# Kernel optimization log

Measured on AMD Instinct MI355X. Metric: run time of the kernel, lower is better.

Reference implementation:

```python
import jax, jax.numpy as jnp
import numpy as np

B, N, D = 2, 1024, 512
H, HD = 8, 64
RPE_IN, RPE_HID = 4, 64
FFN = 2048
EPS = 1e-5


def _layernorm(x, g, b):
    mu = jnp.mean(x, axis=-1, keepdims=True)
    var = jnp.var(x, axis=-1, keepdims=True)
    return (x - mu) * jax.lax.rsqrt(var + EPS) * g + b


def setup_inputs() -> dict:
    key = jax.random.key(0)
    ks = jax.random.split(key, 24)
    s = lambda fan_in: 1.0 / np.sqrt(fan_in)
    # weights stored [in, out] (torch Linear transposed)
    return {
        "x": jax.random.normal(ks[0], (B, N, D), jnp.float32),
        "rel_pos": jax.random.normal(ks[1], (B, N, N, RPE_IN), jnp.float32),
        "Wq": jax.random.uniform(ks[2], (D, D), jnp.float32, -s(D), s(D)),
        "bq": jnp.zeros((D,), jnp.float32),
        "Wk": jax.random.uniform(ks[3], (D, D), jnp.float32, -s(D), s(D)),
        "bk": jnp.zeros((D,), jnp.float32),
        "Wv": jax.random.uniform(ks[4], (D, D), jnp.float32, -s(D), s(D)),
        "bv": jnp.zeros((D,), jnp.float32),
        "Wo": jax.random.uniform(ks[5], (D, D), jnp.float32, -s(D), s(D)),
        "bo": jnp.zeros((D,), jnp.float32),
        "R1": jax.random.uniform(ks[6], (RPE_IN, RPE_HID), jnp.float32, -s(RPE_IN), s(RPE_IN)),
        "rb1": jnp.zeros((RPE_HID,), jnp.float32),
        "R2": jax.random.uniform(ks[7], (RPE_HID, H), jnp.float32, -s(RPE_HID), s(RPE_HID)),
        "rb2": jnp.zeros((H,), jnp.float32),
        "g1": jnp.ones((D,), jnp.float32),
        "b1": jnp.zeros((D,), jnp.float32),
        "g2": jnp.ones((D,), jnp.float32),
        "b2": jnp.zeros((D,), jnp.float32),
        "F1": jax.random.uniform(ks[8], (D, FFN), jnp.float32, -s(D), s(D)),
        "fb1": jnp.zeros((FFN,), jnp.float32),
        "F2": jax.random.uniform(ks[9], (FFN, D), jnp.float32, -s(FFN), s(FFN)),
        "fb2": jnp.zeros((D,), jnp.float32),
    }


def reference(x, rel_pos, Wq, bq, Wk, bk, Wv, bv, Wo, bo,
              R1, rb1, R2, rb2, g1, b1, g2, b2, F1, fb1, F2, fb2):
    scale = 1.0 / np.sqrt(HD)
    q = (x @ Wq + bq).reshape(B, N, H, HD).transpose(0, 2, 1, 3)  # [B,H,N,hd]
    k = (x @ Wk + bk).reshape(B, N, H, HD).transpose(0, 2, 1, 3)
    v = (x @ Wv + bv).reshape(B, N, H, HD).transpose(0, 2, 1, 3)
    attn = jnp.einsum('bhid,bhjd->bhij', q, k) * scale
    rpe = (jax.nn.relu(rel_pos @ R1 + rb1) @ R2 + rb2)  # [B,N,N,H]
    attn = attn + rpe.transpose(0, 3, 1, 2)
    attn = jax.nn.softmax(attn, axis=-1)
    out = jnp.einsum('bhij,bhjd->bhid', attn, v).transpose(0, 2, 1, 3).reshape(B, N, D)
    out = out @ Wo + bo
    x = _layernorm(x + out, g1, b1)
    ffn = jax.nn.gelu(x @ F1 + fb1, approximate=False) @ F2 + fb2
    return _layernorm(x + ffn, g2, b2)
```

## Files before the change

kernel.cpp:

```cpp
#include <hip/hip_runtime.h>
#include <math.h>

#define BATCH 2
#define SEQ   1024
#define DMODEL 512
#define NHEAD 8
#define HDIM  64
#define FFND  2048
#define BH    (BATCH*NHEAD)

typedef float  f32x4  __attribute__((ext_vector_type(4)));
typedef __bf16 bf16x8 __attribute__((ext_vector_type(8)));

#define WAITVM(n) asm volatile("s_waitcnt vmcnt(" #n ")" ::: "memory")

__device__ __forceinline__ unsigned short f2bf(float f) {
  union { __bf16 h; unsigned short u; } z; z.h = (__bf16)f; return z.u;
}
__device__ __forceinline__ float bf2f(unsigned short h) {
  union { unsigned u; float f; } x; x.u = ((unsigned)h) << 16;
  return x.f;
}
__device__ __forceinline__ unsigned pk2(float a, float b) {
  union { __bf16 h[2]; unsigned u; } z;
  z.h[0] = (__bf16)a; z.h[1] = (__bf16)b; return z.u;
}
__device__ __forceinline__ float gelu_f(float v) {
  float u = 0.7978845608f * (v + 0.044715f * v * v * v);
  float a = fabsf(u);
  float e = __expf(-2.f * a);
  float t = (1.f - e) / (1.f + e);
  t = copysignf(t, u);
  return 0.5f * v * (1.f + t);
}

__device__ __forceinline__ void load_lds16(const void* g, void* l) {
  __builtin_amdgcn_global_load_lds((const __attribute__((address_space(1))) void*)g,
                                   (__attribute__((address_space(3))) void*)l, 16, 0, 0);
}

__global__ __launch_bounds__(256) void prep_misc(
    const float* __restrict__ x, const float* __restrict__ bq,
    const float* __restrict__ bk, const float* __restrict__ bv,
    unsigned short* __restrict__ xb, float* __restrict__ bqkv) {
  int gid = blockIdx.x * 256 + threadIdx.x;
  float4 v = ((const float4*)x)[gid];
  ushort4 s;
  s.x = f2bf(v.x); s.y = f2bf(v.y); s.z = f2bf(v.z); s.w = f2bf(v.w);
  ((ushort4*)xb)[gid] = s;
  if (gid < 1536)
    bqkv[gid] = gid < 512 ? bq[gid] : (gid < 1024 ? bk[gid - 512] : bv[gid - 1024]);
}

__global__ __launch_bounds__(256) void prep_weights(
    const float* __restrict__ Wq, const float* __restrict__ Wk,
    const float* __restrict__ Wv, const float* __restrict__ Wo,
    const float* __restrict__ F1, const float* __restrict__ F2,
    unsigned short* __restrict__ qkvT, unsigned short* __restrict__ WoT,
    unsigned short* __restrict__ F1T, unsigned short* __restrict__ F2T) {
  __shared__ float t[32][33];
  int bid = blockIdx.x;
  const float* src; unsigned short* dst; int R, C, tx, ty;
  if (bid < 1024) {
    int m = bid >> 8;
    src = m == 0 ? Wq : m == 1 ? Wk : m == 2 ? Wv : Wo;
    dst = m < 3 ? qkvT + m * 512 * 512 : WoT;
    R = 512; C = 512; int u = bid & 255; tx = u & 15; ty = u >> 4;
  } else if (bid < 2048) {
    src = F1; dst = F1T; R = 512; C = 2048;
    int u = bid - 1024; tx = u & 63; ty = u >> 6;
  } else {
    src = F2; dst = F2T; R = 2048; C = 512;
    int u = bid - 2048; tx = u & 15; ty = u >> 4;
  }
  int c0 = tx * 32, r0 = ty * 32;
  int x_ = threadIdx.x, y_ = threadIdx.y;
#pragma unroll
  for (int i = 0; i < 4; i++)
    t[y_ + i * 8][x_] = src[(size_t)(r0 + y_ + i * 8) * C + c0 + x_];
  __syncthreads();
#pragma unroll
  for (int i = 0; i < 4; i++)
    dst[(size_t)(c0 + y_ + i * 8) * R + r0 + x_] = f2bf(t[x_][y_ + i * 8]);
}

__global__ __launch_bounds__(256) void rpe_mfma(
    const float* __restrict__ rel, const float* __restrict__ R1,
    const float* __restrict__ rb1, const float* __restrict__ R2,
    const float* __restrict__ rb2, unsigned short* __restrict__ rpe) {
  __shared__ unsigned short Hs[4][64 * 64];
  __shared__ unsigned short Os[4][8 * 64];
  const int tid = threadIdx.x, lane = tid & 63, w = tid >> 6;
  const int l15 = lane & 15, l4g = lane >> 4;
  char* Hw = (char*)&Hs[w][0];
  char* Ow = (char*)&Os[w][0];

  bf16x8 a1[4];
#pragma unroll
  for (int mt = 0; mt < 4; mt++) {
    bf16x8 z = {};
    if (l4g == 0) {
      int m = mt * 16 + l15;
      z[0] = (__bf16)R1[0 * 64 + m];
      z[1] = (__bf16)R1[1 * 64 + m];
      z[2] = (__bf16)R1[2 * 64 + m];
      z[3] = (__bf16)R1[3 * 64 + m];
      z[4] = (__bf16)rb1[m];
    }
    a1[mt] = z;
  }
  bf16x8 b2f[2];
#pragma unroll
  for (int ks = 0; ks < 2; ks++) {
    bf16x8 z = {};
    if (l15 < 8) {
#pragma unroll
      for (int j = 0; j < 8; j++)
        z[j] = (__bf16)R2[(ks * 32 + l4g * 8 + j) * 8 + l15];
    }
    b2f[ks] = z;
  }
  float rb2v = (l15 < 8) ? rb2[l15] : 0.f;

  const int nwaves = gridDim.x * 4;
  const int wgid = blockIdx.x * 4 + w;
  for (int itr = 0; itr < 8; itr++) {
    int p0 = (wgid + itr * nwaves) * 64;
    bf16x8 b1[4];
#pragma unroll
    for (int nt = 0; nt < 4; nt++) {
      bf16x8 z = {};
      if (l4g == 0) {
        float4 rv = *(const float4*)&rel[(size_t)(p0 + nt * 16 + l15) * 4];
        z[0] = (__bf16)rv.x; z[1] = (__bf16)rv.y;
        z[2] = (__bf16)rv.z; z[3] = (__bf16)rv.w;
        z[4] = (__bf16)1.0f;
      }
      b1[nt] = z;
    }
#pragma unroll
    for (int nt = 0; nt < 4; nt++) {
#pragma unroll
      for (int mt = 0; mt < 4; mt++) {
        f32x4 hacc = __builtin_amdgcn_mfma_f32_16x16x32_bf16(
            a1[mt], b1[nt], (f32x4){0.f, 0.f, 0.f, 0.f}, 0, 0, 0);
        int row = nt * 16 + l15;
        int dim0 = mt * 16 + l4g * 4;
        float v0 = fmaxf(hacc[0], 0.f);
        float v1 = fmaxf(hacc[1], 0.f);
        float v2 = fmaxf(hacc[2], 0.f);
        float v3 = fmaxf(hacc[3], 0.f);
        int byte = (row * 128 + dim0 * 2) ^ ((row & 7) << 4);
        uint2 pk; pk.x = pk2(v0, v1); pk.y = pk2(v2, v3);
        *(uint2*)(Hw + byte) = pk;
      }
    }
    f32x4 acc2[4];
#pragma unroll
    for (int mt = 0; mt < 4; mt++) acc2[mt] = (f32x4){0.f, 0.f, 0.f, 0.f};
#pragma unroll
    for (int ks = 0; ks < 2; ks++) {
#pragma unroll
      for (int mt = 0; mt < 4; mt++) {
        int row = mt * 16 + l15;
        int byte = (row * 128 + (ks * 32 + l4g * 8) * 2) ^ ((l15 & 7) << 4);
        bf16x8 af = *(const bf16x8*)(Hw + byte);
        acc2[mt] = __builtin_amdgcn_mfma_f32_16x16x32_bf16(af, b2f[ks], acc2[mt], 0, 0, 0);
      }
    }
#pragma unroll
    for (int mt = 0; mt < 4; mt++) {
      if (l15 < 8) {
        int byte = (l15 * 128 + (mt * 16 + l4g * 4) * 2) ^ ((l15 & 7) << 4);
        uint2 pk;
        pk.x = pk2(acc2[mt][0] + rb2v, acc2[mt][1] + rb2v);
        pk.y = pk2(acc2[mt][2] + rb2v, acc2[mt][3] + rb2v);
        *(uint2*)(Ow + byte) = pk;
      }
    }
    {
      int h = lane >> 3, rb = (lane & 7) * 8;
      int byte = (h * 128 + rb * 2) ^ ((h & 7) << 4);
      uint4 ov = *(const uint4*)(Ow + byte);
      int b = p0 >> 20, ij0 = (p0 & 1048575) + rb;
      *(uint4*)&rpe[((size_t)(b * 8 + h) << 20) + ij0] = ov;
    }
  }
}

enum { EPI_F32 = 0, EPI_GELU = 1, EPI_QKV = 2 };

template <int EPI, int BMt, int BNt, int WM, int WN>
__global__ __launch_bounds__(256) void gemm_bt(
    const unsigned short* __restrict__ A, const unsigned short* __restrict__ Bt,
    const float* __restrict__ bias, void* __restrict__ O0, void* __restrict__ O1,
    void* __restrict__ O2, int M, int N, int K) {
  __shared__ unsigned short As[2][BMt * 64];
  __shared__ unsigned short Bs[2][BNt * 64];
  const int tid = threadIdx.x, lane = tid & 63, w = tid >> 6;
  const int wr = w >> 1, wc = w & 1;
  const int m0 = blockIdx.y * BMt, n0 = blockIdx.x * BNt;
  const int l15 = lane & 15, l4g = lane >> 4;
  constexpr int NL = BMt / 32 + BNt / 32;

  f32x4 acc[WM][WN];
#pragma unroll
  for (int i = 0; i < WM; i++)
#pragma unroll
    for (int j = 0; j < WN; j++) acc[i][j] = (f32x4){0.f, 0.f, 0.f, 0.f};

  auto stage = [&](int buf, int kt) {
#pragma unroll
    for (int it = 0; it < BMt / 32; ++it) {
      int c = it * 256 + tid, row = c >> 3;
      int s16 = (c & 7) ^ (row & 7);
      load_lds16(A + (size_t)(m0 + row) * K + kt * 64 + s16 * 8,
                 (char*)&As[buf][0] + c * 16);
    }
#pragma unroll
    for (int it = 0; it < BNt / 32; ++it) {
      int c = it * 256 + tid, row = c >> 3;
      int s16 = (c & 7) ^ (row & 7);
      load_lds16(Bt + (size_t)(n0 + row) * K + kt * 64 + s16 * 8,
                 (char*)&Bs[buf][0] + c * 16);
    }
  };

  const int nkt = K / 64;
  stage(0, 0);
  for (int kt = 0; kt < nkt; ++kt) {
    const int cur = kt & 1;
    if (kt + 1 < nkt) {
      stage(cur ^ 1, kt + 1);
      if constexpr (NL == 6) WAITVM(6); else WAITVM(4);
    } else {
      WAITVM(0);
    }
    __builtin_amdgcn_s_barrier();
#pragma unroll
    for (int kk = 0; kk < 2; ++kk) {
      bf16x8 af[WM], bfv[WN];
#pragma unroll
      for (int i = 0; i < WM; i++) {
        int row = wr * (WM * 16) + i * 16 + l15;
        af[i] = *(const bf16x8*)((char*)&As[cur][0] + row * 128 +
                                 (((kk * 4 + l4g) ^ (row & 7)) << 4));
      }
#pragma unroll
      for (int j = 0; j < WN; j++) {
        int row = wc * (WN * 16) + j * 16 + l15;
        bfv[j] = *(const bf16x8*)((char*)&Bs[cur][0] + row * 128 +
                                  (((kk * 4 + l4g) ^ (row & 7)) << 4));
      }
#pragma unroll
      for (int i = 0; i < WM; i++)
#pragma unroll
        for (int j = 0; j < WN; j++)
          acc[i][j] = __builtin_amdgcn_mfma_f32_16x16x32_bf16(af[i], bfv[j], acc[i][j], 0, 0, 0);
    }
    if (kt + 1 < nkt) {
      asm volatile("" ::: "memory");
      __builtin_amdgcn_s_barrier();
    }
  }

#pragma unroll
  for (int i = 0; i < WM; i++) {
    int row = m0 + wr * (WM * 16) + i * 16 + l4g * 4;
#pragma unroll
    for (int j = 0; j < WN; j++) {
      int col = n0 + wc * (WN * 16) + j * 16 + l15;
      float bv = bias ? bias[col] : 0.f;
#pragma unroll
      for (int r = 0; r < 4; r++) {
        float v = acc[i][j][r] + bv;
        int rr = row + r;
        if (EPI == EPI_F32) {
          ((float*)O0)[(size_t)rr * N + col] = v;
        } else if (EPI == EPI_GELU) {
          ((unsigned short*)O0)[(size_t)rr * N + col] = f2bf(gelu_f(v));
        } else {
          int b = rr >> 10, n = rr & 1023;
          int d = col & 511, h = d >> 6, hd = d & 63;
          int bh = b * 8 + h;
          unsigned short bv16 = f2bf(v);
          if (col < 512)
            ((unsigned short*)O0)[((size_t)bh * 1024 + n) * 64 + hd] = bv16;
          else if (col < 1024)
            ((unsigned short*)O1)[((size_t)bh * 1024 + n) * 64 + hd] = bv16;
          else
            ((unsigned short*)O2)[((size_t)bh * 64 + hd) * 1024 + n] = bv16;
        }
      }
    }
  }
}

__global__ __launch_bounds__(256) void attn_kernel(
    const unsigned short* __restrict__ Qh, const unsigned short* __restrict__ Kh,
    const unsigned short* __restrict__ VT, const unsigned short* __restrict__ rpe,
    unsigned short* __restrict__ AO) {
  __shared__ unsigned short Ks[2][64 * 64], Vs[2][64 * 64], Rs[2][64 * 64];
  __shared__ unsigned short Ps[4][16 * 64];
  const int tid = threadIdx.x, lane = tid & 63, w = tid >> 6;
  const int l15 = lane & 15, l4g = lane >> 4;
  const int bid = blockIdx.x;
  const int it = (bid >> 3) & 15;
  const int bh = (bid & 7) | ((bid >> 7) << 3);
  const int i0 = it * 64;
  const unsigned short* Qb = Qh + (size_t)bh * SEQ * HDIM;
  const unsigned short* Kb = Kh + (size_t)bh * SEQ * HDIM;
  const unsigned short* Vb = VT + (size_t)bh * HDIM * SEQ;
  const unsigned short* Rb = rpe + ((size_t)bh << 20);

  bf16x8 qf[2];
#pragma unroll
  for (int kk = 0; kk < 2; kk++)
    qf[kk] = *(const bf16x8*)&Qb[(size_t)(i0 + w * 16 + l15) * 64 + kk * 32 + l4g * 8];

  f32x4 o[4];
#pragma unroll
  for (int i = 0; i < 4; i++) o[i] = (f32x4){0.f, 0.f, 0.f, 0.f};
  float m4[4], l4s[4];
#pragma unroll
  for (int r = 0; r < 4; r++) { m4[r] = -1e30f; l4s[r] = 0.f; }

  auto stage = [&](int buf, int jt) {
    int j0 = jt * 64;
#pragma unroll
    for (int itn = 0; itn < 2; ++itn) {
      int c = itn * 256 + tid, row = c >> 3;
      int s8 = ((c & 7) ^ (row & 7)) * 8;
      load_lds16(Kb + (size_t)(j0 + row) * 64 + s8, (char*)&Ks[buf][0] + c * 16);
      load_lds16(Vb + (size_t)row * SEQ + j0 + s8, (char*)&Vs[buf][0] + c * 16);
      load_lds16(Rb + (size_t)(i0 + row) * SEQ + j0 + s8, (char*)&Rs[buf][0] + c * 16);
    }
  };

  stage(0, 0);
  for (int jt = 0; jt < 16; ++jt) {
    const int cur = jt & 1;
    if (jt < 15) {
      stage(cur ^ 1, jt + 1);
      WAITVM(6);
    } else {
      WAITVM(0);
    }
    __builtin_amdgcn_s_barrier();

    f32x4 sa[4];
#pragma unroll
    for (int js = 0; js < 4; js++) sa[js] = (f32x4){0.f, 0.f, 0.f, 0.f};
#pragma unroll
    for (int kk = 0; kk < 2; kk++) {
#pragma unroll
      for (int js = 0; js < 4; js++) {
        int row = js * 16 + l15;
        bf16x8 kb = *(const bf16x8*)((char*)&Ks[cur][0] + row * 128 +
                                     (((kk * 4 + l4g) ^ (row & 7)) << 4));
        sa[js] = __builtin_amdgcn_mfma_f32_16x16x32_bf16(qf[kk], kb, sa[js], 0, 0, 0);
      }
    }
    float p[4][4], mx[4];
#pragma unroll
    for (int r = 0; r < 4; r++) mx[r] = -1e30f;
#pragma unroll
    for (int js = 0; js < 4; js++)
#pragma unroll
      for (int r = 0; r < 4; r++) {
        int row = w * 16 + l4g * 4 + r;
        int byte = row * 128 + ((((js * 2) + (l15 >> 3)) ^ (row & 7)) << 4) + ((l15 & 7) << 1);
        float rv = bf2f(*(const unsigned short*)((const char*)&Rs[cur][0] + byte));
        float s = sa[js][r] * 0.125f + rv;
        p[js][r] = s;
        mx[r] = fmaxf(mx[r], s);
      }
#pragma unroll
    for (int off = 1; off < 16; off <<= 1)
#pragma unroll
      for (int r = 0; r < 4; r++) mx[r] = fmaxf(mx[r], __shfl_xor(mx[r], off));
    float al[4], sm[4];
#pragma unroll
    for (int r = 0; r < 4; r++) {
      float nm = fmaxf(m4[r], mx[r]);
      al[r] = __expf(m4[r] - nm);
      m4[r] = nm;
      sm[r] = 0.f;
    }
#pragma unroll
    for (int js = 0; js < 4; js++)
#pragma unroll
      for (int r = 0; r < 4; r++) {
        float e = __expf(p[js][r] - m4[r]);
        p[js][r] = e;
        sm[r] += e;
      }
#pragma unroll
    for (int off = 1; off < 16; off <<= 1)
#pragma unroll
      for (int r = 0; r < 4; r++) sm[r] += __shfl_xor(sm[r], off);
#pragma unroll
    for (int r = 0; r < 4; r++) l4s[r] = l4s[r] * al[r] + sm[r];
#pragma unroll
    for (int hdf = 0; hdf < 4; hdf++)
#pragma unroll
      for (int r = 0; r < 4; r++) o[hdf][r] *= al[r];
#pragma unroll
    for (int js = 0; js < 4; js++)
#pragma unroll
      for (int r = 0; r < 4; r++) {
        int row = l4g * 4 + r;
        int byte = row * 128 + ((((js * 2) + (l15 >> 3)) ^ (row & 7)) << 4) + ((l15 & 7) << 1);
        *(unsigned short*)((char*)&Ps[w][0] + byte) = f2bf(p[js][r]);
      }
#pragma unroll
    for (int kk = 0; kk < 2; kk++) {
      bf16x8 pf = *(const bf16x8*)((char*)&Ps[w][0] + l15 * 128 +
                                   (((kk * 4 + l4g) ^ (l15 & 7)) << 4));
#pragma unroll
      for (int hdf = 0; hdf < 4; hdf++) {
        int row = hdf * 16 + l15;
        bf16x8 vb = *(const bf16x8*)((char*)&Vs[cur][0] + row * 128 +
                                     (((kk * 4 + l4g) ^ (row & 7)) << 4));
        o[hdf] = __builtin_amdgcn_mfma_f32_16x16x32_bf16(pf, vb, o[hdf], 0, 0, 0);
      }
    }
    if (jt < 15) {
      asm volatile("" ::: "memory");
      __builtin_amdgcn_s_barrier();
    }
  }
  const int b = bh >> 3, h = bh & 7;
#pragma unroll
  for (int hdf = 0; hdf < 4; hdf++)
#pragma unroll
    for (int r = 0; r < 4; r++) {
      float v = o[hdf][r] / l4s[r];
      int n = i0 + w * 16 + l4g * 4 + r;
      AO[((size_t)b * SEQ + n) * DMODEL + h * 64 + hdf * 16 + l15] = f2bf(v);
    }
}

__global__ __launch_bounds__(256) void ln_kernel(
    const float* __restrict__ a, const float* __restrict__ res,
    const float* __restrict__ g, const float* __restrict__ be,
    float* __restrict__ outf, unsigned short* __restrict__ outb) {
  const int row = blockIdx.x, t = threadIdx.x;
  const float* pa = a + (size_t)row * DMODEL;
  const float* pb = res + (size_t)row * DMODEL;
  float v0 = pa[t] + pb[t];
  float v1 = pa[t + 256] + pb[t + 256];
  float s = v0 + v1, sq = v0 * v0 + v1 * v1;
#pragma unroll
  for (int off = 1; off < 64; off <<= 1) {
    s += __shfl_xor(s, off);
    sq += __shfl_xor(sq, off);
  }
  __shared__ float ls[4], lq[4];
  int w = t >> 6, lane = t & 63;
  if (lane == 0) { ls[w] = s; lq[w] = sq; }
  __syncthreads();
  s = ls[0] + ls[1] + ls[2] + ls[3];
  sq = lq[0] + lq[1] + lq[2] + lq[3];
  float mu = s * (1.f / DMODEL);
  float var = sq * (1.f / DMODEL) - mu * mu;
  float rs = rsqrtf(var + 1e-5f);
  float y0 = (v0 - mu) * rs * g[t] + be[t];
  float y1v = (v1 - mu) * rs * g[t + 256] + be[t + 256];
  outf[(size_t)row * DMODEL + t] = y0;
  outf[(size_t)row * DMODEL + t + 256] = y1v;
  if (outb) {
    outb[(size_t)row * DMODEL + t] = f2bf(y0);
    outb[(size_t)row * DMODEL + t + 256] = f2bf(y1v);
  }
}

extern "C" void kernel_launch(void* const* d_in, const int* in_sizes, int n_in,
                              void* d_out, int out_size, void* d_ws, size_t ws_size,
                              hipStream_t stream) {
  const float* x   = (const float*)d_in[0];
  const float* rel = (const float*)d_in[1];
  const float* Wq  = (const float*)d_in[2];
  const float* bq  = (const float*)d_in[3];
  const float* Wk  = (const float*)d_in[4];
  const float* bk  = (const float*)d_in[5];
  const float* Wv  = (const float*)d_in[6];
  const float* bv  = (const float*)d_in[7];
  const float* Wo  = (const float*)d_in[8];
  const float* bo  = (const float*)d_in[9];
  const float* R1  = (const float*)d_in[10];
  const float* rb1 = (const float*)d_in[11];
  const float* R2  = (const float*)d_in[12];
  const float* rb2 = (const float*)d_in[13];
  const float* g1  = (const float*)d_in[14];
  const float* b1  = (const float*)d_in[15];
  const float* g2  = (const float*)d_in[16];
  const float* b2  = (const float*)d_in[17];
  const float* F1  = (const float*)d_in[18];
  const float* fb1 = (const float*)d_in[19];
  const float* F2  = (const float*)d_in[20];
  const float* fb2 = (const float*)d_in[21];

  char* p = (char*)d_ws;
  auto alloc = [&](size_t bytes) {
    char* r = p;
    p += (bytes + 255) & ~(size_t)255;
    return r;
  };
  unsigned short* xb   = (unsigned short*)alloc((size_t)2048 * 512 * 2);
  unsigned short* qkvT = (unsigned short*)alloc((size_t)1536 * 512 * 2);
  float*          bqkv = (float*)alloc(1536 * 4);
  unsigned short* WoT  = (unsigned short*)alloc((size_t)512 * 512 * 2);
  unsigned short* F1T  = (unsigned short*)alloc((size_t)2048 * 512 * 2);
  unsigned short* F2T  = (unsigned short*)alloc((size_t)512 * 2048 * 2);
  unsigned short* Qhp  = (unsigned short*)alloc((size_t)BH * SEQ * HDIM * 2);
  unsigned short* Khp  = (unsigned short*)alloc((size_t)BH * SEQ * HDIM * 2);
  unsigned short* VTp  = (unsigned short*)alloc((size_t)BH * HDIM * SEQ * 2);
  unsigned short* rpep = (unsigned short*)alloc((size_t)BH * SEQ * SEQ * 2);
  unsigned short* attO = (unsigned short*)alloc((size_t)2048 * 512 * 2);
  float*          t1   = (float*)alloc((size_t)2048 * 512 * 4);
  float*          y1   = (float*)alloc((size_t)2048 * 512 * 4);
  unsigned short* y1b  = (unsigned short*)alloc((size_t)2048 * 512 * 2);
  float*          t2   = t1;
  unsigned short* hbuf = rpep;

  prep_misc<<<1024, 256, 0, stream>>>(x, bq, bk, bv, xb, bqkv);
  prep_weights<<<3072, dim3(32, 8), 0, stream>>>(Wq, Wk, Wv, Wo, F1, F2,
                                                 qkvT, WoT, F1T, F2T);
  rpe_mfma<<<1024, 256, 0, stream>>>(rel, R1, rb1, R2, rb2, rpep);

  gemm_bt<EPI_QKV, 128, 64, 4, 2><<<dim3(24, 16), 256, 0, stream>>>(
      xb, qkvT, bqkv, Qhp, Khp, VTp, 2048, 1536, 512);
  attn_kernel<<<256, 256, 0, stream>>>(Qhp, Khp, VTp, rpep, attO);

  gemm_bt<EPI_F32, 64, 64, 2, 2><<<dim3(8, 32), 256, 0, stream>>>(
      attO, WoT, bo, t1, nullptr, nullptr, 2048, 512, 512);
  ln_kernel<<<2048, 256, 0, stream>>>(x, t1, g1, b1, y1, y1b);

  gemm_bt<EPI_GELU, 128, 64, 4, 2><<<dim3(32, 16), 256, 0, stream>>>(
      y1b, F1T, fb1, hbuf, nullptr, nullptr, 2048, 2048, 512);
  gemm_bt<EPI_F32, 64, 64, 2, 2><<<dim3(8, 32), 256, 0, stream>>>(
      hbuf, F2T, fb2, t2, nullptr, nullptr, 2048, 512, 2048);
  ln_kernel<<<2048, 256, 0, stream>>>(y1, t2, g2, b2, (float*)d_out, nullptr);
}
```

Before: 251.3 us.

## Use 32x32 MFMA for RPE first layer and prioritize attention MFMA phases

The RPE MLP kernel now handles 32 positions per wave-iteration. The first layer uses a 32x32x16 MFMA instead of many 16x16x32 MFMAs whose K dimension was mostly zero padding, and the grid doubles to 2048 blocks with smaller LDS buffers. This cuts wasted matrix work in the first layer and raises occupancy. The attention kernel also wraps its QK and PV MFMA sections in s_setprio so those waves get scheduling priority over the softmax work of other waves. Output stores in the RPE kernel become 8-byte instead of 16-byte, which may lower write efficiency.

```diff
diff --git a/kernel.cpp b/kernel.cpp
--- a/kernel.cpp
+++ b/kernel.cpp
@@ -9,8 +9,9 @@
 #define FFND  2048
 #define BH    (BATCH*NHEAD)
 
-typedef float  f32x4  __attribute__((ext_vector_type(4)));
-typedef __bf16 bf16x8 __attribute__((ext_vector_type(8)));
+typedef float  f32x4   __attribute__((ext_vector_type(4)));
+typedef float  f32x16  __attribute__((ext_vector_type(16)));
+typedef __bf16 bf16x8  __attribute__((ext_vector_type(8)));
 
 #define WAITVM(n) asm volatile("s_waitcnt vmcnt(" #n ")" ::: "memory")
 
@@ -88,24 +89,25 @@
     const float* __restrict__ rel, const float* __restrict__ R1,
     const float* __restrict__ rb1, const float* __restrict__ R2,
     const float* __restrict__ rb2, unsigned short* __restrict__ rpe) {
-  __shared__ unsigned short Hs[4][64 * 64];
-  __shared__ unsigned short Os[4][8 * 64];
+  __shared__ unsigned short Hs[4][32 * 64];
+  __shared__ unsigned short Os[4][8 * 32];
   const int tid = threadIdx.x, lane = tid & 63, w = tid >> 6;
+  const int l31 = lane & 31, hi = lane >> 5;
   const int l15 = lane & 15, l4g = lane >> 4;
   char* Hw = (char*)&Hs[w][0];
   char* Ow = (char*)&Os[w][0];
 
-  bf16x8 a1[4];
-#pragma unroll
-  for (int mt = 0; mt < 4; mt++) {
+  bf16x8 a1[2];
+#pragma unroll
+  for (int mt = 0; mt < 2; mt++) {
     bf16x8 z = {};
-    if (l4g == 0) {
-      int m = mt * 16 + l15;
-      z[0] = (__bf16)R1[0 * 64 + m];
-      z[1] = (__bf16)R1[1 * 64 + m];
-      z[2] = (__bf16)R1[2 * 64 + m];
-      z[3] = (__bf16)R1[3 * 64 + m];
-      z[4] = (__bf16)rb1[m];
+    if (hi == 0) {
+      int d = mt * 32 + l31;
+      z[0] = (__bf16)R1[0 * 64 + d];
+      z[1] = (__bf16)R1[1 * 64 + d];
+      z[2] = (__bf16)R1[2 * 64 + d];
+      z[3] = (__bf16)R1[3 * 64 + d];
+      z[4] = (__bf16)rb1[d];
     }
     a1[mt] = z;
   }
@@ -122,68 +124,56 @@
   }
   float rb2v = (l15 < 8) ? rb2[l15] : 0.f;
 
-  const int nwaves = gridDim.x * 4;
   const int wgid = blockIdx.x * 4 + w;
-  for (int itr = 0; itr < 8; itr++) {
-    int p0 = (wgid + itr * nwaves) * 64;
-    bf16x8 b1[4];
-#pragma unroll
-    for (int nt = 0; nt < 4; nt++) {
-      bf16x8 z = {};
-      if (l4g == 0) {
-        float4 rv = *(const float4*)&rel[(size_t)(p0 + nt * 16 + l15) * 4];
-        z[0] = (__bf16)rv.x; z[1] = (__bf16)rv.y;
-        z[2] = (__bf16)rv.z; z[3] = (__bf16)rv.w;
-        z[4] = (__bf16)1.0f;
-      }
-      b1[nt] = z;
-    }
-#pragma unroll
-    for (int nt = 0; nt < 4; nt++) {
-#pragma unroll
-      for (int mt = 0; mt < 4; mt++) {
-        f32x4 hacc = __builtin_amdgcn_mfma_f32_16x16x32_bf16(
-            a1[mt], b1[nt], (f32x4){0.f, 0.f, 0.f, 0.f}, 0, 0, 0);
-        int row = nt * 16 + l15;
-        int dim0 = mt * 16 + l4g * 4;
-        float v0 = fmaxf(hacc[0], 0.f);
-        float v1 = fmaxf(hacc[1], 0.f);
-        float v2 = fmaxf(hacc[2], 0.f);
-        float v3 = fmaxf(hacc[3], 0.f);
-        int byte = (row * 128 + dim0 * 2) ^ ((row & 7) << 4);
+  for (int c = 0; c < 8; c++) {
+    int p0 = (wgid + c * 8192) * 32;
+    bf16x8 b1 = {};
+    if (hi == 0) {
+      float4 rv = *(const float4*)&rel[(size_t)(p0 + l31) * 4];
+      b1[0] = (__bf16)rv.x; b1[1] = (__bf16)rv.y;
+      b1[2] = (__bf16)rv.z; b1[3] = (__bf16)rv.w;
+      b1[4] = (__bf16)1.0f;
+    }
+#pragma unroll
+    for (int mt = 0; mt < 2; mt++) {
+      f32x16 hz = {};
+      f32x16 h = __builtin_amdgcn_mfma_f32_32x32x16_bf16(a1[mt], b1, hz, 0, 0, 0);
+#pragma unroll
+      for (int q = 0; q < 4; q++) {
+        float v0 = fmaxf(h[4 * q + 0], 0.f), v1 = fmaxf(h[4 * q + 1], 0.f);
+        float v2 = fmaxf(h[4 * q + 2], 0.f), v3 = fmaxf(h[4 * q + 3], 0.f);
         uint2 pk; pk.x = pk2(v0, v1); pk.y = pk2(v2, v3);
+        int byte = (l31 * 128 + (mt * 32 + q * 8 + hi * 4) * 2) ^ ((l31 & 7) << 4);
         *(uint2*)(Hw + byte) = pk;
       }
     }
-    f32x4 acc2[4];
-#pragma unroll
-    for (int mt = 0; mt < 4; mt++) acc2[mt] = (f32x4){0.f, 0.f, 0.f, 0.f};
-#pragma unroll
-    for (int ks = 0; ks < 2; ks++) {
-#pragma unroll
-      for (int mt = 0; mt < 4; mt++) {
-        int row = mt * 16 + l15;
-        int byte = (row * 128 + (ks * 32 + l4g * 8) * 2) ^ ((l15 & 7) << 4);
+    f32x4 acc2[2];
+    acc2[0] = (f32x4){0.f, 0.f, 0.f, 0.f};
+    acc2[1] = (f32x4){0.f, 0.f, 0.f, 0.f};
+#pragma unroll
+    for (int ks = 0; ks < 2; ks++)
+#pragma unroll
+      for (int mt2 = 0; mt2 < 2; mt2++) {
+        int row = mt2 * 16 + l15;
+        int byte = (row * 128 + (ks * 32 + l4g * 8) * 2) ^ ((row & 7) << 4);
         bf16x8 af = *(const bf16x8*)(Hw + byte);
-        acc2[mt] = __builtin_amdgcn_mfma_f32_16x16x32_bf16(af, b2f[ks], acc2[mt], 0, 0, 0);
-      }
-    }
-#pragma unroll
-    for (int mt = 0; mt < 4; mt++) {
+        acc2[mt2] = __builtin_amdgcn_mfma_f32_16x16x32_bf16(af, b2f[ks], acc2[mt2], 0, 0, 0);
+      }
+#pragma unroll
+    for (int mt2 = 0; mt2 < 2; mt2++) {
       if (l15 < 8) {
-        int byte = (l15 * 128 + (mt * 16 + l4g * 4) * 2) ^ ((l15 & 7) << 4);
         uint2 pk;
-        pk.x = pk2(acc2[mt][0] + rb2v, acc2[mt][1] + rb2v);
-        pk.y = pk2(acc2[mt][2] + rb2v, acc2[mt][3] + rb2v);
+        pk.x = pk2(acc2[mt2][0] + rb2v, acc2[mt2][1] + rb2v);
+        pk.y = pk2(acc2[mt2][2] + rb2v, acc2[mt2][3] + rb2v);
+        int byte = l15 * 64 + (mt2 * 16 + l4g * 4) * 2;
         *(uint2*)(Ow + byte) = pk;
       }
     }
     {
-      int h = lane >> 3, rb = (lane & 7) * 8;
-      int byte = (h * 128 + rb * 2) ^ ((h & 7) << 4);
-      uint4 ov = *(const uint4*)(Ow + byte);
-      int b = p0 >> 20, ij0 = (p0 & 1048575) + rb;
-      *(uint4*)&rpe[((size_t)(b * 8 + h) << 20) + ij0] = ov;
+      int h = lane >> 3, j0 = (lane & 7) * 4;
+      uint2 ov = *(const uint2*)(Ow + h * 64 + j0 * 2);
+      int b = p0 >> 20, ij0 = (p0 & 1048575) + j0;
+      *(uint2*)&rpe[((size_t)(b * 8 + h) << 20) + ij0] = ov;
     }
   }
 }
@@ -351,6 +341,7 @@
     f32x4 sa[4];
 #pragma unroll
     for (int js = 0; js < 4; js++) sa[js] = (f32x4){0.f, 0.f, 0.f, 0.f};
+    __builtin_amdgcn_s_setprio(1);
 #pragma unroll
     for (int kk = 0; kk < 2; kk++) {
 #pragma unroll
@@ -361,6 +352,7 @@
         sa[js] = __builtin_amdgcn_mfma_f32_16x16x32_bf16(qf[kk], kb, sa[js], 0, 0, 0);
       }
     }
+    __builtin_amdgcn_s_setprio(0);
     float p[4][4], mx[4];
 #pragma unroll
     for (int r = 0; r < 4; r++) mx[r] = -1e30f;
@@ -413,6 +405,7 @@
         int byte = row * 128 + ((((js * 2) + (l15 >> 3)) ^ (row & 7)) << 4) + ((l15 & 7) << 1);
         *(unsigned short*)((char*)&Ps[w][0] + byte) = f2bf(p[js][r]);
       }
+    __builtin_amdgcn_s_setprio(1);
 #pragma unroll
     for (int kk = 0; kk < 2; kk++) {
       bf16x8 pf = *(const bf16x8*)((char*)&Ps[w][0] + l15 * 128 +
@@ -425,6 +418,7 @@
         o[hdf] = __builtin_amdgcn_mfma_f32_16x16x32_bf16(pf, vb, o[hdf], 0, 0, 0);
       }
     }
+    __builtin_amdgcn_s_setprio(0);
     if (jt < 15) {
       asm volatile("" ::: "memory");
       __builtin_amdgcn_s_barrier();
@@ -527,7 +521,7 @@
   prep_misc<<<1024, 256, 0, stream>>>(x, bq, bk, bv, xb, bqkv);
   prep_weights<<<3072, dim3(32, 8), 0, stream>>>(Wq, Wk, Wv, Wo, F1, F2,
                                                  qkvT, WoT, F1T, F2T);
-  rpe_mfma<<<1024, 256, 0, stream>>>(rel, R1, rb1, R2, rb2, rpep);
+  rpe_mfma<<<2048, 256, 0, stream>>>(rel, R1, rb1, R2, rb2, rpep);
 
   gemm_bt<EPI_QKV, 128, 64, 4, 2><<<dim3(24, 16), 256, 0, stream>>>(
       xb, qkvT, bqkv, Qhp, Khp, VTp, 2048, 1536, 512);
```

Result: faster. 245.4 us (-2.4%).
